# Optimization experiments

Measured on AMD Instinct MI355X. Metric: run time of the kernel, lower is better.

Reference implementation:

```python
import jax, jax.numpy as jnp
import numpy as np

SCALE = 32 ** (-0.5)  # hardcoded in the original module, independent of head_size

def setup_inputs() -> dict:
    key = jax.random.key(0)
    k1, k2, k3, k4 = jax.random.split(key, 4)
    B, T, E, H = 8, 4096, 2048, 128
    x = jax.random.normal(k1, (B, T, E), dtype=jnp.float32)
    Wq = jax.random.normal(k2, (E, H), dtype=jnp.float32) * (E ** -0.5)
    Wk = jax.random.normal(k3, (E, H), dtype=jnp.float32) * (E ** -0.5)
    Wv = jax.random.normal(k4, (E, H), dtype=jnp.float32) * (E ** -0.5)
    return {"x": x, "Wq": Wq, "Wk": Wk, "Wv": Wv}

def reference(x, Wq, Wk, Wv):
    # q,k,v: [B,T,H]
    q = jnp.einsum('bte,eh->bth', x, Wq)
    k = jnp.einsum('bte,eh->bth', x, Wk)
    v = jnp.einsum('bte,eh->bth', x, Wv)
    # wei: [B, T(query), T(key)]
    wei = jnp.einsum('bqh,bkh->bqk', q, k) * SCALE
    # NOTE: original uses F.softmax(wei, dim=1) -> normalize over the QUERY axis
    wei = jax.nn.softmax(wei, axis=1)
    # dropout prob is 0 in this deterministic baseline (eval mode)
    out = jnp.einsum('bqk,bkh->bqh', wei, v)
    return out
```

## Files before the change

kernel.cpp:

```cpp
#include <hip/hip_runtime.h>
#include <hip/hip_bf16.h>
#include <hip/hip_fp16.h>

#define Bn 8
#define Tn 4096
#define En 2048
#define Hn 128

typedef __attribute__((ext_vector_type(8))) short bf16x8;
typedef __attribute__((ext_vector_type(4))) float f32x4;
typedef __attribute__((ext_vector_type(4))) unsigned int u32x4;

typedef const __attribute__((address_space(1))) unsigned int* gptr_t;
typedef __attribute__((address_space(3))) unsigned int* lptr_t;

static __device__ __forceinline__ void gload16(const void* g, void* l) {
    __builtin_amdgcn_global_load_lds((gptr_t)g, (lptr_t)l, 16, 0, 0);
}

static __device__ __forceinline__ unsigned short f2bf(float f) {
    union { float f; unsigned u; } v; v.f = f;
    unsigned r = v.u + 0x7FFFu + ((v.u >> 16) & 1u);
    return (unsigned short)(r >> 16);
}
static __device__ __forceinline__ float b2f(unsigned short bits) {
    union { unsigned u; float f; } v; v.u = ((unsigned)bits) << 16;
    return v.f;
}
static __device__ __forceinline__ unsigned cvtpk(float lo, float hi) {
    unsigned r;
    asm volatile("v_cvt_pk_bf16_f32 %0, %1, %2" : "=v"(r) : "v"(lo), "v"(hi));
    return r;
}

#define MFMA16(a, b, c) __builtin_amdgcn_mfma_f32_16x16x32_bf16((a), (b), (c), 0, 0, 0)
#define EXP2F(x) __builtin_amdgcn_exp2f(x)
#define WAIT_VM_PUB(N) do { asm volatile("s_waitcnt vmcnt(" #N ")" ::: "memory"); \
                            __builtin_amdgcn_sched_barrier(0); \
                            __builtin_amdgcn_s_barrier(); \
                            __builtin_amdgcn_sched_barrier(0); } while (0)
#define LGKM_BARRIER() do { asm volatile("s_waitcnt lgkmcnt(0)" ::: "memory"); \
                            __builtin_amdgcn_s_barrier(); \
                            __builtin_amdgcn_sched_barrier(0); } while (0)

__global__ __launch_bounds__(256) void prep_w(const float* __restrict__ Wq,
                                              const float* __restrict__ Wk,
                                              const float* __restrict__ Wv,
                                              unsigned short* __restrict__ Wt) {
    int idx = blockIdx.x * 256 + threadIdx.x;
    int w = idx / (En * Hn);
    int rem = idx - w * (En * Hn);
    int kx = rem >> 7;
    int n  = rem & 127;
    const float* W = (w == 0) ? Wq : (w == 1) ? Wk : Wv;
    float f = W[rem];
    if (w == 0) f *= (0.17677669529663687f * 1.4426950408889634f);
    Wt[(size_t)w * En * Hn + (size_t)n * En + kx] = f2bf(f);
}

__global__ __launch_bounds__(256, 2) void qkv_mfma(const float* __restrict__ x,
                                                   const unsigned short* __restrict__ Wt,
                                                   unsigned short* __restrict__ qs,
                                                   unsigned short* __restrict__ ks,
                                                   unsigned short* __restrict__ vT) {
    __shared__ __align__(16) unsigned short Al[2][128][64];
    __shared__ __align__(16) unsigned short Bl[2][128][64];
    const int bid = blockIdx.x;
    const int w = bid % 3;
    const int m0 = (bid / 3) * 128;
    const int b = m0 >> 12;
    const int tb = m0 & (Tn - 1);
    const int t = threadIdx.x;
    const int lane = t & 63, wid = t >> 6;
    const int wr = (wid >> 1) * 64, wc = (wid & 1) * 64;
    const int fr = lane & 15, fq = lane >> 4;
    const unsigned short* Wb = Wt + (size_t)w * En * Hn;
    const int agrp = t >> 4, aln = t & 15;
    const int bR = lane >> 3, bC = lane & 7;

    #pragma unroll
    for (int j = 0; j < 8; ++j) {
        int row = agrp * 8 + j;
        float4 v = *reinterpret_cast<const float4*>(&x[(size_t)(m0 + row) * En + aln * 4]);
        int c = (aln >> 1) ^ ((row ^ (row >> 3)) & 7);
        *reinterpret_cast<uint2*>((char*)&Al[0][0][0] + row * 128 + c * 16 + (aln & 1) * 8)
            = make_uint2(cvtpk(v.x, v.y), cvtpk(v.z, v.w));
    }
    #pragma unroll
    for (int s_ = 0; s_ < 4; ++s_) {
        int seg = wid * 4 + s_;
        int r = seg * 8 + bR;
        gload16(&Wb[(size_t)r * En + ((bC ^ (r & 7)) * 8)],
                (char*)&Bl[0][0][0] + seg * 1024 + lane * 16);
    }
    asm volatile("s_waitcnt vmcnt(0) lgkmcnt(0)" ::: "memory");
    __builtin_amdgcn_s_barrier();
    __builtin_amdgcn_sched_barrier(0);

    f32x4 acc[4][4] = {};
    for (int s = 0; s < 32; ++s) {
        const int cur = s & 1;
        const int kn = ((s + 1) & 31) * 64;
        float4 ar_[8];
        #pragma unroll
        for (int j = 0; j < 8; ++j) {
            int row = agrp * 8 + j;
            ar_[j] = *reinterpret_cast<const float4*>(&x[(size_t)(m0 + row) * En + kn + aln * 4]);
        }
        __builtin_amdgcn_sched_barrier(0);
        #pragma unroll
        for (int s_ = 0; s_ < 4; ++s_) {
            int seg = wid * 4 + s_;
            int r = seg * 8 + bR;
            gload16(&Wb[(size_t)r * En + kn + ((bC ^ (r & 7)) * 8)],
                    (char*)&Bl[cur ^ 1][0][0] + seg * 1024 + lane * 16);
        }
        __builtin_amdgcn_sched_barrier(0);
        #pragma unroll
        for (int ksub = 0; ksub < 2; ++ksub) {
            bf16x8 av[4], bv[4];
            #pragma unroll
            for (int mi = 0; mi < 4; ++mi) {
                int row = wr + mi * 16 + fr;
                int ch = (ksub * 4 + fq) ^ ((row ^ (row >> 3)) & 7);
                av[mi] = *reinterpret_cast<const bf16x8*>(
                    (const char*)&Al[cur][0][0] + row * 128 + ch * 16);
            }
            #pragma unroll
            for (int ni = 0; ni < 4; ++ni) {
                int row = wc + ni * 16 + fr;
                int ch = (ksub * 4 + fq) ^ (row & 7);
                bv[ni] = *reinterpret_cast<const bf16x8*>(
                    (const char*)&Bl[cur][0][0] + row * 128 + ch * 16);
            }
            #pragma unroll
            for (int mi = 0; mi < 4; ++mi)
                #pragma unroll
                for (int ni = 0; ni < 4; ++ni)
                    acc[mi][ni] = MFMA16(av[mi], bv[ni], acc[mi][ni]);
        }
        asm volatile("s_waitcnt vmcnt(4)" ::: "memory");
        __builtin_amdgcn_sched_barrier(0);
        #pragma unroll
        for (int j = 0; j < 8; ++j) {
            int row = agrp * 8 + j;
            int c = (aln >> 1) ^ ((row ^ (row >> 3)) & 7);
            *reinterpret_cast<uint2*>((char*)&Al[cur ^ 1][0][0] + row * 128 + c * 16 + (aln & 1) * 8)
                = make_uint2(cvtpk(ar_[j].x, ar_[j].y), cvtpk(ar_[j].z, ar_[j].w));
        }
        asm volatile("s_waitcnt vmcnt(0) lgkmcnt(0)" ::: "memory");
        __builtin_amdgcn_s_barrier();
        __builtin_amdgcn_sched_barrier(0);
    }

    if (w < 2) {
        unsigned short* out = (w == 0) ? qs : ks;
        #pragma unroll
        for (int mi = 0; mi < 4; ++mi)
            #pragma unroll
            for (int ni = 0; ni < 4; ++ni)
                #pragma unroll
                for (int r = 0; r < 4; ++r) {
                    int row = m0 + wr + mi * 16 + fq * 4 + r;
                    int col = wc + ni * 16 + fr;
                    out[(size_t)row * Hn + col] = f2bf(acc[mi][ni][r]);
                }
    } else {
        #pragma unroll
        for (int mi = 0; mi < 4; ++mi)
            #pragma unroll
            for (int ni = 0; ni < 4; ++ni)
                #pragma unroll
                for (int r = 0; r < 4; ++r) {
                    int tt = tb + wr + mi * 16 + fq * 4 + r;
                    int h  = wc + ni * 16 + fr;
                    vT[((size_t)b * Hn + h) * Tn + tt] = f2bf(acc[mi][ni][r]);
                }
    }
}

__global__ __launch_bounds__(256, 2) void stats_qk(const unsigned short* __restrict__ qs,
                                                   const unsigned short* __restrict__ ks,
                                                   float2* __restrict__ part) {
    __shared__ __align__(16) char smem[65536];
    const int bid = blockIdx.x;
    const int b = bid & 7;
    const int rest = bid >> 3;
    const int kt = rest & 31;
    const int qh = rest >> 5;
    const int k0 = kt * 128;
    const unsigned short* qb = qs + (size_t)b * Tn * Hn;
    const unsigned short* kb = ks + (size_t)b * Tn * Hn;
    const int t = threadIdx.x;
    const int lane = t & 63, wid = t >> 6;
    const int wk = wid >> 1, wq = wid & 1;
    const int fr = lane & 15, fq = lane >> 4;
    const int srow = t >> 4, schk = t & 15;

    #pragma unroll
    for (int it = 0; it < 8; ++it) {
        int r = it * 16 + srow;
        gload16(&kb[(size_t)(k0 + r) * Hn + ((schk ^ (r & 15)) * 8)],
                smem + it * 4096 + t * 16);
    }
    #pragma unroll
    for (int it = 0; it < 4; ++it) {
        int r = it * 16 + srow;
        gload16(&qb[(size_t)(qh * 2048 + r) * Hn + ((schk ^ (r & 15)) * 8)],
                smem + 32768 + it * 4096 + t * 16);
    }
    __syncthreads();
    bf16x8 av[4][4];
    #pragma unroll
    for (int mi = 0; mi < 4; ++mi)
        #pragma unroll
        for (int kc = 0; kc < 4; ++kc) {
            int row = wk * 64 + mi * 16 + fr;
            int ch = (kc * 4 + fq) ^ (row & 15);
            av[mi][kc] = *reinterpret_cast<const bf16x8*>(smem + row * 256 + ch * 16);
        }

    float m[4][4], l[4][4];
    #pragma unroll
    for (int mi = 0; mi < 4; ++mi)
        #pragma unroll
        for (int r = 0; r < 4; ++r) { m[mi][r] = -INFINITY; l[mi][r] = 0.f; }

    for (int step = 0; step < 32; ++step) {
        const int cur = step & 1;
        const int qn = qh * 2048 + ((step + 1) & 31) * 64;
        #pragma unroll
        for (int it = 0; it < 4; ++it) {
            int r = it * 16 + srow;
            gload16(&qb[(size_t)(qn + r) * Hn + ((schk ^ (r & 15)) * 8)],
                    smem + 32768 + (cur ^ 1) * 16384 + it * 4096 + t * 16);
        }
        WAIT_VM_PUB(4);
        const char* Qc = smem + 32768 + cur * 16384;
        f32x4 acc[4][2] = {};
        __builtin_amdgcn_s_setprio(1);
        #pragma unroll
        for (int kc = 0; kc < 4; ++kc) {
            bf16x8 bv[2];
            #pragma unroll
            for (int ni = 0; ni < 2; ++ni) {
                int row = wq * 32 + ni * 16 + fr;
                int ch = (kc * 4 + fq) ^ (row & 15);
                bv[ni] = *reinterpret_cast<const bf16x8*>(Qc + row * 256 + ch * 16);
            }
            #pragma unroll
            for (int mi = 0; mi < 4; ++mi)
                #pragma unroll
                for (int ni = 0; ni < 2; ++ni)
                    acc[mi][ni] = MFMA16(av[mi][kc], bv[ni], acc[mi][ni]);
        }
        __builtin_amdgcn_s_setprio(0);
        #pragma unroll
        for (int mi = 0; mi < 4; ++mi)
            #pragma unroll
            for (int r = 0; r < 4; ++r) {
                float v0 = acc[mi][0][r], v1 = acc[mi][1][r];
                float mn = fmaxf(m[mi][r], fmaxf(v0, v1));
                l[mi][r] = l[mi][r] * EXP2F(m[mi][r] - mn) + EXP2F(v0 - mn) + EXP2F(v1 - mn);
                m[mi][r] = mn;
            }
        LGKM_BARRIER();
    }
    #pragma unroll
    for (int off = 1; off <= 8; off <<= 1) {
        #pragma unroll
        for (int mi = 0; mi < 4; ++mi)
            #pragma unroll
            for (int r = 0; r < 4; ++r) {
                float mo = __shfl_xor(m[mi][r], off);
                float lo = __shfl_xor(l[mi][r], off);
                float mn = fmaxf(m[mi][r], mo);
                l[mi][r] = l[mi][r] * EXP2F(m[mi][r] - mn) + lo * EXP2F(mo - mn);
                m[mi][r] = mn;
            }
    }
    if (fr == 0) {
        #pragma unroll
        for (int mi = 0; mi < 4; ++mi)
            #pragma unroll
            for (int r = 0; r < 4; ++r) {
                int k = k0 + wk * 64 + mi * 16 + fq * 4 + r;
                part[((size_t)b * Tn + k) * 4 + qh * 2 + wq] = make_float2(m[mi][r], l[mi][r]);
            }
    }
}

__global__ __launch_bounds__(256) void stats_comb(const float2* __restrict__ part,
                                                  float* __restrict__ mr) {
    int g = blockIdx.x * 256 + threadIdx.x;
    const float2* pp = part + (size_t)g * 4;
    float2 p0 = pp[0], p1 = pp[1], p2 = pp[2], p3 = pp[3];
    float M = fmaxf(fmaxf(p0.x, p1.x), fmaxf(p2.x, p3.x));
    float L = p0.y * EXP2F(p0.x - M) + p1.y * EXP2F(p1.x - M) +
              p2.y * EXP2F(p2.x - M) + p3.y * EXP2F(p3.x - M);
    mr[g] = M + __log2f(L);
}

__global__ __launch_bounds__(256) void scale_v(const unsigned short* __restrict__ vT,
                                               const float* __restrict__ mr,
                                               unsigned short* __restrict__ vn) {
    size_t i = ((size_t)blockIdx.x * 256 + threadIdx.x) * 8;
    int t0 = (int)(i & (Tn - 1));
    int b = (int)(i >> 19);
    const float* mrb = mr + (size_t)b * Tn + t0;
    ushort4 v0 = *reinterpret_cast<const ushort4*>(vT + i);
    ushort4 v1 = *reinterpret_cast<const ushort4*>(vT + i + 4);
    float4 s0 = *reinterpret_cast<const float4*>(mrb);
    float4 s1 = *reinterpret_cast<const float4*>(mrb + 4);
    unsigned o[4];
    o[0] = cvtpk(b2f(v0.x) * EXP2F(-s0.x), b2f(v0.y) * EXP2F(-s0.y));
    o[1] = cvtpk(b2f(v0.z) * EXP2F(-s0.z), b2f(v0.w) * EXP2F(-s0.w));
    o[2] = cvtpk(b2f(v1.x) * EXP2F(-s1.x), b2f(v1.y) * EXP2F(-s1.y));
    o[3] = cvtpk(b2f(v1.z) * EXP2F(-s1.z), b2f(v1.w) * EXP2F(-s1.w));
    *reinterpret_cast<u32x4*>(vn + i) = *reinterpret_cast<u32x4*>(o);
}

__global__ __launch_bounds__(256, 2) void attn_pv(const unsigned short* __restrict__ qs,
                                                  const unsigned short* __restrict__ ks,
                                                  const unsigned short* __restrict__ vn,
                                                  float* __restrict__ opart) {
    __shared__ __align__(16) char smem[81920];
    const int bid = blockIdx.x;
    const int b = bid & 7;
    const int rest = bid >> 3;
    const int qp = rest & 31;
    const int kh = rest >> 5;
    const int kbase = kh * 2048;
    const unsigned short* qg = qs + (size_t)b * Tn * Hn;
    const unsigned short* kg = ks + (size_t)b * Tn * Hn;
    const unsigned short* vg = vn + (size_t)b * Hn * Tn;
    const int t = threadIdx.x;
    const int lane = t & 63, wid = t >> 6;
    const int wk = wid >> 1, wq = wid & 1;
    const int fr = lane & 15, fq = lane >> 4;
    const int srow16 = t >> 4, schk16 = t & 15;
    const int srow8 = t >> 3, schk8 = t & 7;

    bf16x8 bq[2][2][4];
    #pragma unroll
    for (int qt = 0; qt < 2; ++qt) {
        int qb0 = qp * 64 + qt * 2048;
        #pragma unroll
        for (int ni = 0; ni < 2; ++ni)
            #pragma unroll
            for (int kc = 0; kc < 4; ++kc) {
                int row = qb0 + wq * 32 + ni * 16 + fr;
                bq[qt][ni][kc] = *reinterpret_cast<const bf16x8*>(
                    &qg[(size_t)row * Hn + kc * 32 + fq * 8]);
            }
    }
    #pragma unroll
    for (int it = 0; it < 4; ++it) {
        int r = it * 16 + srow16;
        gload16(&kg[(size_t)(kbase + r) * Hn + ((schk16 ^ (r & 15)) * 8)],
                smem + it * 4096 + t * 16);
        int rv = it * 32 + srow8;
        gload16(&vg[(size_t)rv * Tn + kbase + ((schk8 ^ (rv & 7)) * 8)],
                smem + 32768 + it * 4096 + t * 16);
    }
    __syncthreads();

    f32x4 acc_o[2][4][2] = {};
    for (int s = 0; s < 32; ++s) {
        const int cur = s & 1;
        {
            const int knr = kbase + ((s + 1) & 31) * 64;
            #pragma unroll
            for (int it = 0; it < 4; ++it) {
                int r = it * 16 + srow16;
                gload16(&kg[(size_t)(knr + r) * Hn + ((schk16 ^ (r & 15)) * 8)],
                        smem + (cur ^ 1) * 16384 + it * 4096 + t * 16);
                int rv = it * 32 + srow8;
                gload16(&vg[(size_t)rv * Tn + knr + ((schk8 ^ (rv & 7)) * 8)],
                        smem + 32768 + (cur ^ 1) * 16384 + it * 4096 + t * 16);
            }
        }
        WAIT_VM_PUB(8);
        const char* Kc = smem + cur * 16384;
        #pragma unroll
        for (int qt = 0; qt < 2; ++qt) {
            char* Pb = smem + 65536 + qt * 8192;
            f32x4 acc_s[2][2] = {};
            __builtin_amdgcn_s_setprio(1);
            #pragma unroll
            for (int kc = 0; kc < 4; ++kc) {
                bf16x8 avk[2];
                #pragma unroll
                for (int mi = 0; mi < 2; ++mi) {
                    int row = wk * 32 + mi * 16 + fr;
                    int ch = (kc * 4 + fq) ^ (row & 15);
                    avk[mi] = *reinterpret_cast<const bf16x8*>(Kc + row * 256 + ch * 16);
                }
                #pragma unroll
                for (int mi = 0; mi < 2; ++mi)
                    #pragma unroll
                    for (int ni = 0; ni < 2; ++ni)
                        acc_s[mi][ni] = MFMA16(avk[mi], bq[qt][ni][kc], acc_s[mi][ni]);
            }
            __builtin_amdgcn_s_setprio(0);
            #pragma unroll
            for (int mi = 0; mi < 2; ++mi)
                #pragma unroll
                for (int ni = 0; ni < 2; ++ni) {
                    float e0 = EXP2F(acc_s[mi][ni][0]);
                    float e1 = EXP2F(acc_s[mi][ni][1]);
                    float e2 = EXP2F(acc_s[mi][ni][2]);
                    float e3 = EXP2F(acc_s[mi][ni][3]);
                    int q = wq * 32 + ni * 16 + fr;
                    int chunk = (wk * 4 + mi * 2 + (fq >> 1)) ^ (q & 7);
                    *reinterpret_cast<uint2*>(Pb + q * 128 + chunk * 16 + (fq & 1) * 8) =
                        make_uint2(cvtpk(e0, e1), cvtpk(e2, e3));
                }
        }
        LGKM_BARRIER();
        const char* Vc = smem + 32768 + cur * 16384;
        __builtin_amdgcn_s_setprio(1);
        #pragma unroll
        for (int kc = 0; kc < 2; ++kc) {
            bf16x8 bp[2][2];
            #pragma unroll
            for (int qt = 0; qt < 2; ++qt)
                #pragma unroll
                for (int ni = 0; ni < 2; ++ni) {
                    int qrow = wq * 32 + ni * 16 + fr;
                    int ch = (kc * 4 + fq) ^ (qrow & 7);
                    bp[qt][ni] = *reinterpret_cast<const bf16x8*>(
                        smem + 65536 + qt * 8192 + qrow * 128 + ch * 16);
                }
            #pragma unroll
            for (int mi = 0; mi < 4; ++mi) {
                int row = wk * 64 + mi * 16 + fr;
                int ch = (kc * 4 + fq) ^ (row & 7);
                bf16x8 avv = *reinterpret_cast<const bf16x8*>(Vc + row * 128 + ch * 16);
                #pragma unroll
                for (int qt = 0; qt < 2; ++qt)
                    #pragma unroll
                    for (int ni = 0; ni < 2; ++ni)
                        acc_o[qt][mi][ni] = MFMA16(avv, bp[qt][ni], acc_o[qt][mi][ni]);
            }
        }
        __builtin_amdgcn_s_setprio(0);
        LGKM_BARRIER();
    }

    float* Ol = (float*)smem;
    __syncthreads();
    float* op = opart + (size_t)kh * Bn * Tn * Hn + (size_t)b * Tn * Hn;
    #pragma unroll
    for (int qt = 0; qt < 2; ++qt) {
        #pragma unroll
        for (int mi = 0; mi < 4; ++mi)
            #pragma unroll
            for (int ni = 0; ni < 2; ++ni) {
                int q = wq * 32 + ni * 16 + fr;
                int h = wk * 64 + mi * 16 + fq * 4;
                *reinterpret_cast<float4*>(&Ol[q * 132 + h]) =
                    make_float4(acc_o[qt][mi][ni][0], acc_o[qt][mi][ni][1],
                                acc_o[qt][mi][ni][2], acc_o[qt][mi][ni][3]);
            }
        __syncthreads();
        int qrow0 = qp * 64 + qt * 2048;
        #pragma unroll
        for (int j = 0; j < 8; ++j) {
            int idx = j * 256 + t;
            int row = idx >> 5, c = (idx & 31) * 4;
            *reinterpret_cast<float4*>(&op[(size_t)(qrow0 + row) * Hn + c]) =
                *reinterpret_cast<const float4*>(&Ol[row * 132 + c]);
        }
        __syncthreads();
    }
}

__global__ __launch_bounds__(256) void combine(const float* __restrict__ opart,
                                               float* __restrict__ out) {
    size_t i = ((size_t)blockIdx.x * 256 + threadIdx.x) * 4;
    const size_t half = (size_t)Bn * Tn * Hn;
    float4 a = *reinterpret_cast<const float4*>(opart + i);
    float4 b = *reinterpret_cast<const float4*>(opart + half + i);
    *reinterpret_cast<float4*>(out + i) =
        make_float4(a.x + b.x, a.y + b.y, a.z + b.z, a.w + b.w);
}

extern "C" void kernel_launch(void* const* d_in, const int* in_sizes, int n_in,
                              void* d_out, int out_size, void* d_ws, size_t ws_size,
                              hipStream_t stream) {
    const float* x  = (const float*)d_in[0];
    const float* Wq = (const float*)d_in[1];
    const float* Wk = (const float*)d_in[2];
    const float* Wv = (const float*)d_in[3];
    float* out = (float*)d_out;

    char* p = (char*)d_ws;
    unsigned short* qs = (unsigned short*)p; p += (size_t)Bn * Tn * Hn * 2;
    unsigned short* ks = (unsigned short*)p; p += (size_t)Bn * Tn * Hn * 2;
    unsigned short* vT = (unsigned short*)p; p += (size_t)Bn * Tn * Hn * 2;
    unsigned short* vn = (unsigned short*)p; p += (size_t)Bn * Tn * Hn * 2;
    unsigned short* Wt = (unsigned short*)p; p += (size_t)3 * En * Hn * 2;
    float2* part       = (float2*)p;         p += (size_t)Bn * Tn * 4 * sizeof(float2);
    float* mr          = (float*)p;          p += (size_t)Bn * Tn * sizeof(float);
    float* opart       = (float*)p;          p += (size_t)2 * Bn * Tn * Hn * sizeof(float);
    size_t needed = (size_t)(p - (char*)d_ws);
    if (ws_size < needed) return;

    prep_w<<<dim3(3 * En * Hn / 256), dim3(256), 0, stream>>>(Wq, Wk, Wv, Wt);
    qkv_mfma<<<dim3((Bn * Tn / 128) * 3), dim3(256), 0, stream>>>(x, Wt, qs, ks, vT);
    stats_qk<<<dim3(512), dim3(256), 0, stream>>>(qs, ks, part);
    stats_comb<<<dim3(Bn * Tn / 256), dim3(256), 0, stream>>>(part, mr);
    scale_v<<<dim3((size_t)Bn * Hn * Tn / (256 * 8)), dim3(256), 0, stream>>>(vT, mr, vn);
    attn_pv<<<dim3(512), dim3(256), 0, stream>>>(qs, ks, vn, opart);
    combine<<<dim3((size_t)Bn * Tn * Hn / (256 * 4)), dim3(256), 0, stream>>>(opart, out);
}
```

Before: 288.1 us.

## Fuse Q/K/V projections into one 128x384-tile GEMM block to read x once

The QKV projection now computes all three weight matrices in one block with a 128x384 output tile and 512 threads, replacing three separate blocks per row tile that each reloaded and converted the same x rows. This cuts global reads of the fp32 input (the dominant traffic, 256 MB) to a third and removes the redundant fp32-to-bf16 conversions. It also wraps the MFMA section in s_setprio and simplifies the LDS swizzle. The trade-off is more LDS per block (about 112 KB), which may limit occupancy to one block per CU, and fewer blocks in the grid (256).

Measured after the change: 240.4 us. 16.5% less time.

```diff
diff --git a/kernel.cpp b/kernel.cpp
--- a/kernel.cpp
+++ b/kernel.cpp
@@ -58,77 +58,77 @@
     Wt[(size_t)w * En * Hn + (size_t)n * En + kx] = f2bf(f);
 }
 
-__global__ __launch_bounds__(256, 2) void qkv_mfma(const float* __restrict__ x,
-                                                   const unsigned short* __restrict__ Wt,
-                                                   unsigned short* __restrict__ qs,
-                                                   unsigned short* __restrict__ ks,
-                                                   unsigned short* __restrict__ vT) {
+__global__ __launch_bounds__(512, 2) void qkv_fused(const float* __restrict__ x,
+                                                    const unsigned short* __restrict__ Wt,
+                                                    unsigned short* __restrict__ qs,
+                                                    unsigned short* __restrict__ ks,
+                                                    unsigned short* __restrict__ vT) {
     __shared__ __align__(16) unsigned short Al[2][128][64];
-    __shared__ __align__(16) unsigned short Bl[2][128][64];
-    const int bid = blockIdx.x;
-    const int w = bid % 3;
-    const int m0 = (bid / 3) * 128;
+    __shared__ __align__(16) unsigned short Bl[2][384][64];
+    const int m0 = blockIdx.x * 128;
     const int b = m0 >> 12;
     const int tb = m0 & (Tn - 1);
     const int t = threadIdx.x;
     const int lane = t & 63, wid = t >> 6;
-    const int wr = (wid >> 1) * 64, wc = (wid & 1) * 64;
+    const int wm = wid >> 2, wn = wid & 3;
     const int fr = lane & 15, fq = lane >> 4;
-    const unsigned short* Wb = Wt + (size_t)w * En * Hn;
     const int agrp = t >> 4, aln = t & 15;
     const int bR = lane >> 3, bC = lane & 7;
 
-    #pragma unroll
-    for (int j = 0; j < 8; ++j) {
-        int row = agrp * 8 + j;
-        float4 v = *reinterpret_cast<const float4*>(&x[(size_t)(m0 + row) * En + aln * 4]);
-        int c = (aln >> 1) ^ ((row ^ (row >> 3)) & 7);
-        *reinterpret_cast<uint2*>((char*)&Al[0][0][0] + row * 128 + c * 16 + (aln & 1) * 8)
-            = make_uint2(cvtpk(v.x, v.y), cvtpk(v.z, v.w));
-    }
-    #pragma unroll
-    for (int s_ = 0; s_ < 4; ++s_) {
-        int seg = wid * 4 + s_;
-        int r = seg * 8 + bR;
-        gload16(&Wb[(size_t)r * En + ((bC ^ (r & 7)) * 8)],
-                (char*)&Bl[0][0][0] + seg * 1024 + lane * 16);
+    {
+        #pragma unroll
+        for (int j = 0; j < 4; ++j) {
+            int row = agrp * 4 + j;
+            float4 v = *reinterpret_cast<const float4*>(&x[(size_t)(m0 + row) * En + aln * 4]);
+            int cb = (aln >> 1) ^ (row & 7);
+            *reinterpret_cast<uint2*>((char*)&Al[0][0][0] + row * 128 + cb * 16 + (aln & 1) * 8)
+                = make_uint2(cvtpk(v.x, v.y), cvtpk(v.z, v.w));
+        }
+        #pragma unroll
+        for (int s_ = 0; s_ < 6; ++s_) {
+            int seg = wid * 6 + s_;
+            int r = seg * 8 + bR;
+            gload16(&Wt[(size_t)r * En + ((bC ^ (r & 7)) * 8)],
+                    (char*)&Bl[0][0][0] + seg * 1024 + lane * 16);
+        }
     }
     asm volatile("s_waitcnt vmcnt(0) lgkmcnt(0)" ::: "memory");
     __builtin_amdgcn_s_barrier();
     __builtin_amdgcn_sched_barrier(0);
 
-    f32x4 acc[4][4] = {};
+    f32x4 acc[4][6] = {};
     for (int s = 0; s < 32; ++s) {
         const int cur = s & 1;
         const int kn = ((s + 1) & 31) * 64;
-        float4 ar_[8];
-        #pragma unroll
-        for (int j = 0; j < 8; ++j) {
-            int row = agrp * 8 + j;
+        float4 ar_[4];
+        #pragma unroll
+        for (int j = 0; j < 4; ++j) {
+            int row = agrp * 4 + j;
             ar_[j] = *reinterpret_cast<const float4*>(&x[(size_t)(m0 + row) * En + kn + aln * 4]);
         }
         __builtin_amdgcn_sched_barrier(0);
         #pragma unroll
-        for (int s_ = 0; s_ < 4; ++s_) {
-            int seg = wid * 4 + s_;
+        for (int s_ = 0; s_ < 6; ++s_) {
+            int seg = wid * 6 + s_;
             int r = seg * 8 + bR;
-            gload16(&Wb[(size_t)r * En + kn + ((bC ^ (r & 7)) * 8)],
+            gload16(&Wt[(size_t)r * En + kn + ((bC ^ (r & 7)) * 8)],
                     (char*)&Bl[cur ^ 1][0][0] + seg * 1024 + lane * 16);
         }
         __builtin_amdgcn_sched_barrier(0);
+        __builtin_amdgcn_s_setprio(1);
         #pragma unroll
         for (int ksub = 0; ksub < 2; ++ksub) {
-            bf16x8 av[4], bv[4];
+            bf16x8 av[4], bv[6];
             #pragma unroll
             for (int mi = 0; mi < 4; ++mi) {
-                int row = wr + mi * 16 + fr;
-                int ch = (ksub * 4 + fq) ^ ((row ^ (row >> 3)) & 7);
+                int row = wm * 64 + mi * 16 + fr;
+                int ch = (ksub * 4 + fq) ^ (row & 7);
                 av[mi] = *reinterpret_cast<const bf16x8*>(
                     (const char*)&Al[cur][0][0] + row * 128 + ch * 16);
             }
             #pragma unroll
-            for (int ni = 0; ni < 4; ++ni) {
-                int row = wc + ni * 16 + fr;
+            for (int ni = 0; ni < 6; ++ni) {
+                int row = wn * 96 + ni * 16 + fr;
                 int ch = (ksub * 4 + fq) ^ (row & 7);
                 bv[ni] = *reinterpret_cast<const bf16x8*>(
                     (const char*)&Bl[cur][0][0] + row * 128 + ch * 16);
@@ -136,16 +136,17 @@
             #pragma unroll
             for (int mi = 0; mi < 4; ++mi)
                 #pragma unroll
-                for (int ni = 0; ni < 4; ++ni)
+                for (int ni = 0; ni < 6; ++ni)
                     acc[mi][ni] = MFMA16(av[mi], bv[ni], acc[mi][ni]);
         }
-        asm volatile("s_waitcnt vmcnt(4)" ::: "memory");
+        __builtin_amdgcn_s_setprio(0);
+        asm volatile("s_waitcnt vmcnt(6)" ::: "memory");
         __builtin_amdgcn_sched_barrier(0);
         #pragma unroll
-        for (int j = 0; j < 8; ++j) {
-            int row = agrp * 8 + j;
-            int c = (aln >> 1) ^ ((row ^ (row >> 3)) & 7);
-            *reinterpret_cast<uint2*>((char*)&Al[cur ^ 1][0][0] + row * 128 + c * 16 + (aln & 1) * 8)
+        for (int j = 0; j < 4; ++j) {
+            int row = agrp * 4 + j;
+            int cb = (aln >> 1) ^ (row & 7);
+            *reinterpret_cast<uint2*>((char*)&Al[cur ^ 1][0][0] + row * 128 + cb * 16 + (aln & 1) * 8)
                 = make_uint2(cvtpk(ar_[j].x, ar_[j].y), cvtpk(ar_[j].z, ar_[j].w));
         }
         asm volatile("s_waitcnt vmcnt(0) lgkmcnt(0)" ::: "memory");
@@ -153,30 +154,21 @@
         __builtin_amdgcn_sched_barrier(0);
     }
 
-    if (w < 2) {
-        unsigned short* out = (w == 0) ? qs : ks;
-        #pragma unroll
-        for (int mi = 0; mi < 4; ++mi)
-            #pragma unroll
-            for (int ni = 0; ni < 4; ++ni)
-                #pragma unroll
-                for (int r = 0; r < 4; ++r) {
-                    int row = m0 + wr + mi * 16 + fq * 4 + r;
-                    int col = wc + ni * 16 + fr;
-                    out[(size_t)row * Hn + col] = f2bf(acc[mi][ni][r]);
-                }
-    } else {
-        #pragma unroll
-        for (int mi = 0; mi < 4; ++mi)
-            #pragma unroll
-            for (int ni = 0; ni < 4; ++ni)
-                #pragma unroll
-                for (int r = 0; r < 4; ++r) {
-                    int tt = tb + wr + mi * 16 + fq * 4 + r;
-                    int h  = wc + ni * 16 + fr;
-                    vT[((size_t)b * Hn + h) * Tn + tt] = f2bf(acc[mi][ni][r]);
-                }
-    }
+    #pragma unroll
+    for (int mi = 0; mi < 4; ++mi)
+        #pragma unroll
+        for (int ni = 0; ni < 6; ++ni) {
+            int c = wn * 96 + ni * 16 + fr;
+            int w = c >> 7, h = c & 127;
+            #pragma unroll
+            for (int r = 0; r < 4; ++r) {
+                int rloc = wm * 64 + mi * 16 + fq * 4 + r;
+                unsigned short val = f2bf(acc[mi][ni][r]);
+                if (w == 0)      qs[(size_t)(m0 + rloc) * Hn + h] = val;
+                else if (w == 1) ks[(size_t)(m0 + rloc) * Hn + h] = val;
+                else             vT[((size_t)b * Hn + h) * Tn + tb + rloc] = val;
+            }
+        }
 }
 
 __global__ __launch_bounds__(256, 2) void stats_qk(const unsigned short* __restrict__ qs,
@@ -508,7 +500,7 @@
     if (ws_size < needed) return;
 
     prep_w<<<dim3(3 * En * Hn / 256), dim3(256), 0, stream>>>(Wq, Wk, Wv, Wt);
-    qkv_mfma<<<dim3((Bn * Tn / 128) * 3), dim3(256), 0, stream>>>(x, Wt, qs, ks, vT);
+    qkv_fused<<<dim3(Bn * Tn / 128), dim3(512), 0, stream>>>(x, Wt, qs, ks, vT);
     stats_qk<<<dim3(512), dim3(256), 0, stream>>>(qs, ks, part);
     stats_comb<<<dim3(Bn * Tn / 256), dim3(256), 0, stream>>>(part, mr);
     scale_v<<<dim3((size_t)Bn * Hn * Tn / (256 * 8)), dim3(256), 0, stream>>>(vT, mr, vn);
```
